# Performance work log

Hardware: AMD Instinct MI355X
Metric: run time of the kernel (lower is better)

The kernel has to match this reference:

```python
import jax, jax.numpy as jnp
import numpy as np

B, L, C = 4, 2048, 1024

def setup_inputs() -> dict:
    key = jax.random.key(0)
    k1, k2, k3 = jax.random.split(key, 3)
    net_in = jax.random.normal(k1, (B, L, C), dtype=jnp.float32)
    # torch Linear weights stored as (out, in); we keep that convention
    w_qkv = jax.random.normal(k2, (3 * C, C), dtype=jnp.float32) * (1.0 / np.sqrt(C))
    w_out = jax.random.normal(k3, (C, C), dtype=jnp.float32) * (1.0 / np.sqrt(C))
    return {"net_in": net_in, "w_qkv": w_qkv, "w_out": w_out}

def reference(net_in, w_qkv, w_out):
    Bc, Lc, Cc = net_in.shape
    qkv = jnp.einsum('blc,dc->bld', net_in, w_qkv)  # (B, L, 3C)
    q, k, v = jnp.split(qkv, 3, axis=-1)
    attn = jnp.einsum('bqc,bkc->bqk', q, k) / jnp.sqrt(jnp.float32(Cc))
    causal = jnp.tril(jnp.ones((Lc, Lc), dtype=bool))
    attn = jnp.where(causal[None, :, :], attn, -jnp.inf)
    attn = jax.nn.softmax(attn, axis=-1)
    out = jnp.einsum('bqk,bkc->bqc', attn, v)
    return jnp.einsum('blc,dc->bld', out, w_out)
```

## Files before the change

kernel.cpp:

```cpp
#include <hip/hip_runtime.h>
#include <hip/hip_bf16.h>
#include <cstdint>
#include <cstddef>

typedef __hip_bfloat16 bf16;
typedef float  floatx4 __attribute__((ext_vector_type(4)));
typedef __bf16 bf16x8  __attribute__((ext_vector_type(8)));

typedef __attribute__((address_space(1))) void as1_void;
typedef __attribute__((address_space(3))) void as3_void;

constexpr int Bn = 4, Ln = 2048, Cn = 1024;

__device__ __forceinline__ void store_one(float* p, float v) { *p = v; }
__device__ __forceinline__ void store_one(bf16*  p, float v) { *p = __float2bfloat16(v); }

#define BAR()    asm volatile("s_barrier" ::: "memory")
#define VMCNT2() asm volatile("s_waitcnt vmcnt(2)" ::: "memory")
#define VMCNT0() asm volatile("s_waitcnt vmcnt(0)" ::: "memory")
#define SCHEDB() __builtin_amdgcn_sched_barrier(0)
#define STAGE(gp, off) \
    __builtin_amdgcn_global_load_lds((const as1_void*)(gp), (as3_void*)(smem + (off)), 16, 0, 0)

template <typename OutT>
__device__ __forceinline__ void gemm256(
    const bf16* __restrict__ A, const bf16* __restrict__ B, OutT* __restrict__ C,
    int m0, int n0, int Keff, int lda, int ldb, int ldc, float cscale)
{
    __shared__ __align__(16) char smem[131072];

    const int tid  = threadIdx.x;
    const int lane = tid & 63;
    const int quad = lane >> 4;
    const int lr   = lane & 15;
    const int wave = tid >> 6;
    const int wm   = (wave >> 2) * 128;
    const int wn   = (wave & 3) * 64;

    floatx4 acc[8][4];
#pragma unroll
    for (int i = 0; i < 8; ++i)
#pragma unroll
        for (int j = 0; j < 4; ++j) { floatx4 z = {0.f, 0.f, 0.f, 0.f}; acc[i][j] = z; }

    const int srow = tid >> 3;
    const int sx   = (tid & 7) ^ (srow & 7);
    const bf16* gA = A + (size_t)(m0 + srow) * lda + sx * 8;
    const bf16* gB = B + (size_t)(n0 + srow) * ldb + sx * 8;
    const int wuni = __builtin_amdgcn_readfirstlane((tid & 0x1C0) * 16);

    const int aoff = (wm + lr) * 64;
    const int boff = (wn + lr) * 64;
    const int s0   = (quad ^ (lr & 7)) * 8;

    const int NT = Keff >> 6;

    STAGE(gB,            32768 + 0 * 8192 + wuni);
    STAGE(gB + 64  * ldb, 32768 + 1 * 8192 + wuni);
    STAGE(gB + 128 * ldb, 32768 + 2 * 8192 + wuni);
    STAGE(gB + 192 * ldb, 32768 + 3 * 8192 + wuni);
    STAGE(gA,                     0 * 8192 + wuni);
    STAGE(gA + 128 * lda,         2 * 8192 + wuni);
    STAGE(gA + 64  * lda,         1 * 8192 + wuni);
    STAGE(gA + 192 * lda,         3 * 8192 + wuni);
    VMCNT2();
    BAR();

#define LDA4(MB, SK) do { _Pragma("unroll") for (int ii = 0; ii < 4; ++ii) \
        a[ii] = *(const bf16x8*)(As + aoff + ((MB) * 4 + ii) * 1024 + (SK)); } while (0)
#define LDB4(SK) do { _Pragma("unroll") for (int nn = 0; nn < 4; ++nn) \
        b[nn] = *(const bf16x8*)(Bs + boff + nn * 1024 + (SK)); } while (0)
#define MFMA16(MB) do { _Pragma("unroll") for (int ii = 0; ii < 4; ++ii) { \
        _Pragma("unroll") for (int nn = 0; nn < 4; ++nn) \
            acc[(MB) * 4 + ii][nn] = __builtin_amdgcn_mfma_f32_16x16x32_bf16( \
                a[ii], b[nn], acc[(MB) * 4 + ii][nn], 0, 0, 0); } } while (0)

    for (int t = 0; t < NT; ++t) {
        const bf16* As = (const bf16*)(smem + (t & 1) * 65536);
        const bf16* Bs = (const bf16*)(smem + (t & 1) * 65536 + 32768);
        const int  wl  = ((t + 1) & 1) * 65536;
        const int  kn  = (t + 1) << 6;
        const bool more = (t + 1 < NT);
        bf16x8 a[4], b[4];

        LDB4(s0);
        LDA4(0, s0);
        if (more) {
            STAGE(gB + kn,            wl + 32768 + 0 * 8192 + wuni);
            STAGE(gB + kn + 64 * ldb, wl + 32768 + 1 * 8192 + wuni);
        }
        BAR(); SCHEDB();
        __builtin_amdgcn_s_setprio(1);
        MFMA16(0);
        __builtin_amdgcn_s_setprio(0);
        SCHEDB();
        if (more) VMCNT2(); else VMCNT0();
        BAR();

        LDA4(1, s0);
        if (more) {
            STAGE(gB + kn + 128 * ldb, wl + 32768 + 2 * 8192 + wuni);
            STAGE(gB + kn + 192 * ldb, wl + 32768 + 3 * 8192 + wuni);
        }
        BAR(); SCHEDB();
        __builtin_amdgcn_s_setprio(1);
        MFMA16(1);
        __builtin_amdgcn_s_setprio(0);
        SCHEDB();
        BAR();

        LDB4(s0 ^ 32);
        LDA4(0, s0 ^ 32);
        if (more) {
            STAGE(gA + kn,             wl + 0 * 8192 + wuni);
            STAGE(gA + kn + 128 * lda, wl + 2 * 8192 + wuni);
        }
        BAR(); SCHEDB();
        __builtin_amdgcn_s_setprio(1);
        MFMA16(0);
        __builtin_amdgcn_s_setprio(0);
        SCHEDB();
        BAR();

        LDA4(1, s0 ^ 32);
        if (more) {
            STAGE(gA + kn + 64  * lda, wl + 1 * 8192 + wuni);
            STAGE(gA + kn + 192 * lda, wl + 3 * 8192 + wuni);
        }
        BAR(); SCHEDB();
        __builtin_amdgcn_s_setprio(1);
        MFMA16(1);
        __builtin_amdgcn_s_setprio(0);
        SCHEDB();
        if (more) VMCNT2();
        BAR();
    }
#undef LDA4
#undef LDB4
#undef MFMA16

#pragma unroll
    for (int mi = 0; mi < 8; ++mi) {
        const int row = m0 + wm + mi * 16 + quad * 4;
#pragma unroll
        for (int n = 0; n < 4; ++n) {
            const int col = n0 + wn + n * 16 + lr;
            OutT* cp = C + (size_t)row * ldc + col;
#pragma unroll
            for (int r = 0; r < 4; ++r)
                store_one(cp + (size_t)r * ldc, acc[mi][n][r] * cscale);
        }
    }
}

__global__ __launch_bounds__(512, 2)
void g1_qk(const bf16* __restrict__ Xb, const bf16* __restrict__ Wqkb,
           bf16* __restrict__ QK)
{
    const int i = blockIdx.x;
    const int j = i >> 3;
    const int mt = (i & 7) * 4 + (j & 3);
    const int nt = j >> 2;
    gemm256<bf16>(Xb, Wqkb, QK, mt * 256, nt * 256, 1024, 1024, 1024, 2048, 1.0f);
}

__global__ __launch_bounds__(512, 2)
void g2_s_w2(const bf16* __restrict__ QK, const bf16* __restrict__ Wob,
             const bf16* __restrict__ WvT, bf16* __restrict__ S,
             bf16* __restrict__ W2)
{
    const int i = blockIdx.x;
    if (i < 144) {
        const int b = (i & 7) >> 1;
        const int t = (i >> 3) * 2 + (i & 1);
        int ti = (int)((sqrtf(8.f * t + 1.f) - 1.f) * 0.5f);
        while ((ti + 1) * (ti + 2) / 2 <= t) ++ti;
        while (ti * (ti + 1) / 2 > t) --ti;
        const int tj = t - ti * (ti + 1) / 2;
        const bf16* Aq = QK + (size_t)b * Ln * 2048;
        const bf16* Bk = Aq + 1024;
        bf16* Sb = S + (size_t)b * Ln * Ln;
        gemm256<bf16>(Aq, Bk, Sb, ti * 256, tj * 256, 1024, 2048, 2048, Ln, 0.03125f);
    } else {
        const int j = i - 144;
        gemm256<bf16>(Wob, WvT, W2, (j & 3) * 256, (j >> 2) * 256, 1024, 1024, 1024, 1024, 1.0f);
    }
}

__device__ __forceinline__ float waveMax(float x) {
#pragma unroll
    for (int o = 32; o > 0; o >>= 1) x = fmaxf(x, __shfl_xor(x, o, 64));
    return x;
}
__device__ __forceinline__ float waveSum(float x) {
#pragma unroll
    for (int o = 32; o > 0; o >>= 1) x += __shfl_xor(x, o, 64);
    return x;
}

__device__ void softmax_rows(bf16* __restrict__ S, int row0)
{
    const int wave = threadIdx.x >> 6, lane = threadIdx.x & 63;
    for (int it8 = 0; it8 < 8; ++it8) {
        const int row = row0 + wave * 8 + it8;
        const int q = row & (Ln - 1);
        bf16* Srow = S + (size_t)row * Ln;
        const int kmax = ((q >> 7) + 1) << 7;
        const int nv = (kmax + 511) >> 9;
        float x[4][8];
        float m = -1e30f;
        for (int it = 0; it < nv; ++it) {
            int c0 = it * 512 + lane * 8;
            bf16x8 v = *(const bf16x8*)(Srow + c0);
#pragma unroll
            for (int e = 0; e < 8; ++e) {
                float f = (float)v[e];
                f = (c0 + e <= q) ? f : -1e30f;
                x[it][e] = f;
                m = fmaxf(m, f);
            }
        }
        m = waveMax(m);
        float s = 0.f;
        for (int it = 0; it < nv; ++it)
#pragma unroll
            for (int e = 0; e < 8; ++e) {
                float ex = (x[it][e] > -1e29f) ? __expf(x[it][e] - m) : 0.f;
                x[it][e] = ex;
                s += ex;
            }
        s = waveSum(s);
        const float inv = 1.f / s;
        for (int it = 0; it < nv; ++it) {
            bf16x8 o;
#pragma unroll
            for (int e = 0; e < 8; ++e) o[e] = (__bf16)(x[it][e] * inv);
            *(bf16x8*)(Srow + it * 512 + lane * 8) = o;
        }
    }
}

__global__ __launch_bounds__(512, 2)
void g3_vwt_sm(const bf16* __restrict__ W2, const bf16* __restrict__ Xb,
               bf16* __restrict__ VWT, bf16* __restrict__ S)
{
    const int i = blockIdx.x;
    if (i < 128) {
        const int j = i >> 3;
        const int nt = (i & 7) * 4 + (j & 3);
        const int mt = j >> 2;
        gemm256<bf16>(W2, Xb, VWT, mt * 256, nt * 256, 1024, 1024, 1024, 8192, 1.0f);
    } else {
        softmax_rows(S, (i - 128) * 64);
    }
}

__global__ __launch_bounds__(512, 2)
void g4_out(const bf16* __restrict__ P, const bf16* __restrict__ VWT,
            float* __restrict__ out)
{
    const int i = blockIdx.x;
    const int b = (i & 7) >> 1, p = i & 1;
    const int q = i >> 3;
    const int mt = q >> 1, nt = p * 2 + (q & 1);
    const bf16* Pp = P + (size_t)b * Ln * Ln;
    const bf16* Bv = VWT + (size_t)b * Ln;
    float* Co = out + (size_t)b * Ln * Cn;
    gemm256<float>(Pp, Bv, Co, mt * 256, nt * 256, (mt + 1) * 256, Ln, 8192, Cn, 1.0f);
}

__global__ __launch_bounds__(256)
void cast_all(const float* __restrict__ X, const float* __restrict__ Wqkv,
              const float* __restrict__ Wo,
              bf16* __restrict__ Xb, bf16* __restrict__ Wqkb,
              bf16* __restrict__ Wob, bf16* __restrict__ WvT)
{
    int blk = blockIdx.x;
    if (blk < 11264) {
        int i = blk * 256 + threadIdx.x;
        const float* src; bf16* dst; int off;
        if (i < 2097152)                 { src = X;    dst = Xb;   off = i; }
        else if (i < 2097152 + 524288)   { src = Wqkv; dst = Wqkb; off = i - 2097152; }
        else                             { src = Wo;   dst = Wob;  off = i - 2621440; }
        float4 f = ((const float4*)src)[off];
        bf16 o0 = __float2bfloat16(f.x), o1 = __float2bfloat16(f.y);
        bf16 o2 = __float2bfloat16(f.z), o3 = __float2bfloat16(f.w);
        ushort4 u;
        u.x = *(unsigned short*)&o0; u.y = *(unsigned short*)&o1;
        u.z = *(unsigned short*)&o2; u.w = *(unsigned short*)&o3;
        *(ushort4*)(dst + (size_t)off * 4) = u;
    } else {
        __shared__ float t[32][33];
        int tt = blk - 11264;
        int c0 = (tt & 31) * 32;
        int r0 = (tt >> 5) * 32;
        const float* Wv = Wqkv + 2048 * 1024;
        int xcol = threadIdx.x & 31, y0 = threadIdx.x >> 5;
#pragma unroll
        for (int p = 0; p < 4; ++p) {
            int y = y0 + 8 * p;
            t[y][xcol] = Wv[(size_t)(r0 + y) * 1024 + c0 + xcol];
        }
        __syncthreads();
#pragma unroll
        for (int p = 0; p < 4; ++p) {
            int mloc = y0 + 8 * p;
            WvT[(size_t)(c0 + mloc) * 1024 + r0 + xcol] = __float2bfloat16(t[xcol][mloc]);
        }
    }
}

extern "C" void kernel_launch(void* const* d_in, const int* in_sizes, int n_in,
                              void* d_out, int out_size, void* d_ws, size_t ws_size,
                              hipStream_t stream)
{
    const float* X    = (const float*)d_in[0];
    const float* Wqkv = (const float*)d_in[1];
    const float* Wout = (const float*)d_in[2];
    float* out = (float*)d_out;

    char* ws = (char*)d_ws;
    const size_t MiB = 1024ull * 1024ull;
    bf16* Xb   = (bf16*)(ws + 0);
    bf16* QK   = (bf16*)(ws + 16 * MiB);
    bf16* VWT  = (bf16*)(ws + 48 * MiB);
    bf16* Sbuf = (bf16*)(ws + 64 * MiB);
    bf16* Wqkb = (bf16*)(ws + 96 * MiB);
    bf16* WvT  = (bf16*)(ws + 100 * MiB);
    bf16* Wob  = (bf16*)(ws + 102 * MiB);
    bf16* W2   = (bf16*)(ws + 104 * MiB);

    cast_all<<<dim3(12288), 256, 0, stream>>>(X, Wqkv, Wout, Xb, Wqkb, Wob, WvT);

    g1_qk<<<dim3(256), 512, 0, stream>>>(Xb, Wqkb, QK);

    g2_s_w2<<<dim3(160), 512, 0, stream>>>(QK, Wob, WvT, Sbuf, W2);

    g3_vwt_sm<<<dim3(256), 512, 0, stream>>>(W2, Xb, VWT, Sbuf);

    g4_out<<<dim3(128), 512, 0, stream>>>(Sbuf, VWT, out);
}
```

Measured before the change: 239.8 us.

## Split-K balance causal P·V GEMM with ticketed partial-sum reduction

The final causal attention-output GEMM had very unbalanced work per tile, since row tile mt has K length (mt+1)*256. It now launches 224 blocks: short rows are paired into one block, and long rows are split along K into 2-3 chunks. Chunk producers write fp32 partials to a scratch buffer that reuses the Xb region, then signal an atomic ticket; the consumer spins until the other chunks arrive and adds them in. This adds scratch traffic and a spin-wait that depends on co-residency of blocks, and tickets are reset inside the cast kernel.

```diff
diff --git a/kernel.cpp b/kernel.cpp
--- a/kernel.cpp
+++ b/kernel.cpp
@@ -22,13 +22,12 @@
 #define STAGE(gp, off) \
     __builtin_amdgcn_global_load_lds((const as1_void*)(gp), (as3_void*)(smem + (off)), 16, 0, 0)
 
-template <typename OutT>
-__device__ __forceinline__ void gemm256(
-    const bf16* __restrict__ A, const bf16* __restrict__ B, OutT* __restrict__ C,
-    int m0, int n0, int Keff, int lda, int ldb, int ldc, float cscale)
-{
-    __shared__ __align__(16) char smem[131072];
-
+__device__ __forceinline__ void gemm256_core(
+    char* __restrict__ smem,
+    const bf16* __restrict__ A, const bf16* __restrict__ B,
+    int m0, int n0, int kbeg, int kend, int lda, int ldb,
+    floatx4 (&acc)[8][4])
+{
     const int tid  = threadIdx.x;
     const int lane = tid & 63;
     const int quad = lane >> 4;
@@ -37,7 +36,6 @@
     const int wm   = (wave >> 2) * 128;
     const int wn   = (wave & 3) * 64;
 
-    floatx4 acc[8][4];
 #pragma unroll
     for (int i = 0; i < 8; ++i)
 #pragma unroll
@@ -45,17 +43,17 @@
 
     const int srow = tid >> 3;
     const int sx   = (tid & 7) ^ (srow & 7);
-    const bf16* gA = A + (size_t)(m0 + srow) * lda + sx * 8;
-    const bf16* gB = B + (size_t)(n0 + srow) * ldb + sx * 8;
+    const bf16* gA = A + (size_t)(m0 + srow) * lda + sx * 8 + kbeg;
+    const bf16* gB = B + (size_t)(n0 + srow) * ldb + sx * 8 + kbeg;
     const int wuni = __builtin_amdgcn_readfirstlane((tid & 0x1C0) * 16);
 
     const int aoff = (wm + lr) * 64;
     const int boff = (wn + lr) * 64;
     const int s0   = (quad ^ (lr & 7)) * 8;
 
-    const int NT = Keff >> 6;
-
-    STAGE(gB,            32768 + 0 * 8192 + wuni);
+    const int NT = (kend - kbeg) >> 6;
+
+    STAGE(gB,             32768 + 0 * 8192 + wuni);
     STAGE(gB + 64  * ldb, 32768 + 1 * 8192 + wuni);
     STAGE(gB + 128 * ldb, 32768 + 2 * 8192 + wuni);
     STAGE(gB + 192 * ldb, 32768 + 3 * 8192 + wuni);
@@ -138,6 +136,23 @@
 #undef LDA4
 #undef LDB4
 #undef MFMA16
+}
+
+template <typename OutT>
+__device__ __forceinline__ void gemm256(
+    char* __restrict__ smem,
+    const bf16* __restrict__ A, const bf16* __restrict__ B, OutT* __restrict__ C,
+    int m0, int n0, int kbeg, int kend, int lda, int ldb, int ldc, float cscale)
+{
+    floatx4 acc[8][4];
+    gemm256_core(smem, A, B, m0, n0, kbeg, kend, lda, ldb, acc);
+
+    const int lane = threadIdx.x & 63;
+    const int quad = lane >> 4;
+    const int lr   = lane & 15;
+    const int wave = threadIdx.x >> 6;
+    const int wm   = (wave >> 2) * 128;
+    const int wn   = (wave & 3) * 64;
 
 #pragma unroll
     for (int mi = 0; mi < 8; ++mi) {
@@ -157,11 +172,12 @@
 void g1_qk(const bf16* __restrict__ Xb, const bf16* __restrict__ Wqkb,
            bf16* __restrict__ QK)
 {
+    __shared__ __align__(16) char smem[131072];
     const int i = blockIdx.x;
     const int j = i >> 3;
     const int mt = (i & 7) * 4 + (j & 3);
     const int nt = j >> 2;
-    gemm256<bf16>(Xb, Wqkb, QK, mt * 256, nt * 256, 1024, 1024, 1024, 2048, 1.0f);
+    gemm256<bf16>(smem, Xb, Wqkb, QK, mt * 256, nt * 256, 0, 1024, 1024, 1024, 2048, 1.0f);
 }
 
 __global__ __launch_bounds__(512, 2)
@@ -169,6 +185,7 @@
              const bf16* __restrict__ WvT, bf16* __restrict__ S,
              bf16* __restrict__ W2)
 {
+    __shared__ __align__(16) char smem[131072];
     const int i = blockIdx.x;
     if (i < 144) {
         const int b = (i & 7) >> 1;
@@ -180,10 +197,10 @@
         const bf16* Aq = QK + (size_t)b * Ln * 2048;
         const bf16* Bk = Aq + 1024;
         bf16* Sb = S + (size_t)b * Ln * Ln;
-        gemm256<bf16>(Aq, Bk, Sb, ti * 256, tj * 256, 1024, 2048, 2048, Ln, 0.03125f);
+        gemm256<bf16>(smem, Aq, Bk, Sb, ti * 256, tj * 256, 0, 1024, 2048, 2048, Ln, 0.03125f);
     } else {
         const int j = i - 144;
-        gemm256<bf16>(Wob, WvT, W2, (j & 3) * 256, (j >> 2) * 256, 1024, 1024, 1024, 1024, 1.0f);
+        gemm256<bf16>(smem, Wob, WvT, W2, (j & 3) * 256, (j >> 2) * 256, 0, 1024, 1024, 1024, 1024, 1.0f);
     }
 }
 
@@ -244,38 +261,128 @@
 void g3_vwt_sm(const bf16* __restrict__ W2, const bf16* __restrict__ Xb,
                bf16* __restrict__ VWT, bf16* __restrict__ S)
 {
+    __shared__ __align__(16) char smem[131072];
     const int i = blockIdx.x;
     if (i < 128) {
         const int j = i >> 3;
         const int nt = (i & 7) * 4 + (j & 3);
         const int mt = j >> 2;
-        gemm256<bf16>(W2, Xb, VWT, mt * 256, nt * 256, 1024, 1024, 1024, 8192, 1.0f);
+        gemm256<bf16>(smem, W2, Xb, VWT, mt * 256, nt * 256, 0, 1024, 1024, 1024, 8192, 1.0f);
     } else {
         softmax_rows(S, (i - 128) * 64);
     }
 }
 
+__device__ const short jb_mt[14]   = {0, 2, 3, 3,   4, 4,   5, 5,   6, 6,    6,    7, 7,    7};
+__device__ const short jb_kb[14]   = {0, 0, 0, 512, 0, 768, 0, 768, 0, 768,  1280, 0, 768,  1536};
+__device__ const short jb_ke[14]   = {0, 768, 512, 1024, 768, 1280, 768, 1536, 768, 1280, 1792, 768, 1536, 2048};
+__device__ const short jb_role[14] = {0, 0, 2, 1,   2, 1,   2, 1,   2, 1,    1,    2, 1,    1};
+__device__ const short jb_cid[14]  = {0, 0, 0, 1,   0, 1,   0, 1,   0, 1,    2,    0, 1,    2};
+__device__ const short jb_nch[14]  = {1, 1, 2, 2,   2, 2,   2, 2,   3, 3,    3,    3, 3,    3};
+
 __global__ __launch_bounds__(512, 2)
 void g4_out(const bf16* __restrict__ P, const bf16* __restrict__ VWT,
-            float* __restrict__ out)
-{
+            float* __restrict__ out, float* __restrict__ paux,
+            int* __restrict__ tickets)
+{
+    __shared__ __align__(16) char smem[131072];
     const int i = blockIdx.x;
-    const int b = (i & 7) >> 1, p = i & 1;
+    const int r = i & 7;
+    const int b = r >> 1, p = r & 1;
     const int q = i >> 3;
-    const int mt = q >> 1, nt = p * 2 + (q & 1);
+    const int nt = p * 2 + (q & 1);
+    const int j = q >> 1;
+
     const bf16* Pp = P + (size_t)b * Ln * Ln;
     const bf16* Bv = VWT + (size_t)b * Ln;
     float* Co = out + (size_t)b * Ln * Cn;
-    gemm256<float>(Pp, Bv, Co, mt * 256, nt * 256, (mt + 1) * 256, Ln, 8192, Cn, 1.0f);
+    const int n0 = nt * 256;
+
+    if (j == 0) {
+        gemm256<float>(smem, Pp, Bv, Co, 0,   n0, 0, 256, Ln, 8192, Cn, 1.0f);
+        gemm256<float>(smem, Pp, Bv, Co, 256, n0, 0, 512, Ln, 8192, Cn, 1.0f);
+        return;
+    }
+
+    const int mt   = jb_mt[j];
+    const int kb   = jb_kb[j];
+    const int ke   = jb_ke[j];
+    const int role = jb_role[j];
+    const int m0   = mt * 256;
+
+    if (role == 0) {
+        gemm256<float>(smem, Pp, Bv, Co, m0, n0, kb, ke, Ln, 8192, Cn, 1.0f);
+        return;
+    }
+
+    floatx4 acc[8][4];
+    gemm256_core(smem, Pp, Bv, m0, n0, kb, ke, Ln, 8192, acc);
+
+    const int tid  = threadIdx.x;
+    const int lane = tid & 63;
+    const int quad = lane >> 4;
+    const int lr   = lane & 15;
+    const int wave = tid >> 6;
+    const int wm   = (wave >> 2) * 128;
+    const int wn   = (wave & 3) * 64;
+
+    const int tred = (b * 4 + nt) * 5 + (mt - 3);
+    float* slot0 = paux + ((size_t)(tred * 2) << 16);
+
+    if (role == 1) {
+        const int cid = jb_cid[j];
+        float* slot = slot0 + ((size_t)(cid - 1) << 16);
+#pragma unroll
+        for (int mi = 0; mi < 8; ++mi) {
+            const int lrow = wm + mi * 16 + quad * 4;
+#pragma unroll
+            for (int n = 0; n < 4; ++n) {
+                const int lcol = wn + n * 16 + lr;
+#pragma unroll
+                for (int rr = 0; rr < 4; ++rr)
+                    slot[(size_t)(lrow + rr) * 256 + lcol] = acc[mi][n][rr];
+            }
+        }
+        __threadfence();
+        __syncthreads();
+        if (tid == 0)
+            __hip_atomic_fetch_add(&tickets[tred], 1, __ATOMIC_RELEASE, __HIP_MEMORY_SCOPE_AGENT);
+        return;
+    }
+
+    const int nch = jb_nch[j];
+    if (tid == 0) {
+        while (__hip_atomic_load(&tickets[tred], __ATOMIC_ACQUIRE, __HIP_MEMORY_SCOPE_AGENT) < nch - 1)
+            __builtin_amdgcn_s_sleep(8);
+    }
+    __syncthreads();
+    const float* s1 = slot0 + 65536;
+#pragma unroll
+    for (int mi = 0; mi < 8; ++mi) {
+        const int lrow = wm + mi * 16 + quad * 4;
+#pragma unroll
+        for (int n = 0; n < 4; ++n) {
+            const int lcol = wn + n * 16 + lr;
+#pragma unroll
+            for (int rr = 0; rr < 4; ++rr) {
+                const size_t li = (size_t)(lrow + rr) * 256 + lcol;
+                float v = acc[mi][n][rr] + slot0[li];
+                if (nch == 3) v += s1[li];
+                Co[(size_t)(m0 + lrow + rr) * Cn + n0 + lcol] = v;
+            }
+        }
+    }
 }
 
 __global__ __launch_bounds__(256)
 void cast_all(const float* __restrict__ X, const float* __restrict__ Wqkv,
               const float* __restrict__ Wo,
               bf16* __restrict__ Xb, bf16* __restrict__ Wqkb,
-              bf16* __restrict__ Wob, bf16* __restrict__ WvT)
+              bf16* __restrict__ Wob, bf16* __restrict__ WvT,
+              int* __restrict__ tickets)
 {
     int blk = blockIdx.x;
+    if (blk == 0 && threadIdx.x < 128) tickets[threadIdx.x] = 0;
     if (blk < 11264) {
         int i = blk * 256 + threadIdx.x;
         const float* src; bf16* dst; int off;
@@ -329,8 +436,10 @@
     bf16* WvT  = (bf16*)(ws + 100 * MiB);
     bf16* Wob  = (bf16*)(ws + 102 * MiB);
     bf16* W2   = (bf16*)(ws + 104 * MiB);
-
-    cast_all<<<dim3(12288), 256, 0, stream>>>(X, Wqkv, Wout, Xb, Wqkb, Wob, WvT);
+    float* paux = (float*)(ws + 0);
+    int* tickets = (int*)(ws + 106 * MiB);
+
+    cast_all<<<dim3(12288), 256, 0, stream>>>(X, Wqkv, Wout, Xb, Wqkb, Wob, WvT, tickets);
 
     g1_qk<<<dim3(256), 512, 0, stream>>>(Xb, Wqkb, QK);
 
@@ -338,5 +447,5 @@
 
     g3_vwt_sm<<<dim3(256), 512, 0, stream>>>(W2, Xb, VWT, Sbuf);
 
-    g4_out<<<dim3(128), 512, 0, stream>>>(Sbuf, VWT, out);
-}
+    g4_out<<<dim3(224), 512, 0, stream>>>(Sbuf, VWT, out, paux, tickets);
+}
```

Result: slower. 327.3 us (+36.5%).

## Shrink GEMM tiles to 128x128 and redistribute work across more blocks

Applied to the files above, without the earlier changes.

Replaces the 256x256 GEMM tile with a 128x128 tile, using 64KB of shared memory and a simpler staging schedule that waits on all loads each k-step. Grids grow four-fold, with new tile-index swizzles, and occupancy rises to 4 blocks per CU. Softmax now runs in every g3 block after its GEMM instead of in separate blocks. The goal is better load balance and CU fill on the small causal and triangular grids, at the cost of lower operand reuse per tile and more global traffic.

```diff
diff --git a/kernel.cpp b/kernel.cpp
--- a/kernel.cpp
+++ b/kernel.cpp
@@ -16,32 +16,30 @@
 __device__ __forceinline__ void store_one(bf16*  p, float v) { *p = __float2bfloat16(v); }
 
 #define BAR()    asm volatile("s_barrier" ::: "memory")
-#define VMCNT2() asm volatile("s_waitcnt vmcnt(2)" ::: "memory")
 #define VMCNT0() asm volatile("s_waitcnt vmcnt(0)" ::: "memory")
 #define SCHEDB() __builtin_amdgcn_sched_barrier(0)
 #define STAGE(gp, off) \
     __builtin_amdgcn_global_load_lds((const as1_void*)(gp), (as3_void*)(smem + (off)), 16, 0, 0)
 
 template <typename OutT>
-__device__ __forceinline__ void gemm256(
+__device__ __forceinline__ void gemm128(
+    char* __restrict__ smem,
     const bf16* __restrict__ A, const bf16* __restrict__ B, OutT* __restrict__ C,
-    int m0, int n0, int Keff, int lda, int ldb, int ldc, float cscale)
-{
-    __shared__ __align__(16) char smem[131072];
-
+    int m0, int n0, int kend, int lda, int ldb, int ldc, float cscale)
+{
     const int tid  = threadIdx.x;
     const int lane = tid & 63;
     const int quad = lane >> 4;
     const int lr   = lane & 15;
     const int wave = tid >> 6;
-    const int wm   = (wave >> 2) * 128;
-    const int wn   = (wave & 3) * 64;
-
-    floatx4 acc[8][4];
-#pragma unroll
-    for (int i = 0; i < 8; ++i)
-#pragma unroll
-        for (int j = 0; j < 4; ++j) { floatx4 z = {0.f, 0.f, 0.f, 0.f}; acc[i][j] = z; }
+    const int wm   = (wave >> 2) * 64;
+    const int wn   = (wave & 3) * 32;
+
+    floatx4 acc[4][2];
+#pragma unroll
+    for (int i = 0; i < 4; ++i)
+#pragma unroll
+        for (int j = 0; j < 2; ++j) { floatx4 z = {0.f, 0.f, 0.f, 0.f}; acc[i][j] = z; }
 
     const int srow = tid >> 3;
     const int sx   = (tid & 7) ^ (srow & 7);
@@ -53,97 +51,82 @@
     const int boff = (wn + lr) * 64;
     const int s0   = (quad ^ (lr & 7)) * 8;
 
-    const int NT = Keff >> 6;
-
-    STAGE(gB,            32768 + 0 * 8192 + wuni);
-    STAGE(gB + 64  * ldb, 32768 + 1 * 8192 + wuni);
-    STAGE(gB + 128 * ldb, 32768 + 2 * 8192 + wuni);
-    STAGE(gB + 192 * ldb, 32768 + 3 * 8192 + wuni);
-    STAGE(gA,                     0 * 8192 + wuni);
-    STAGE(gA + 128 * lda,         2 * 8192 + wuni);
-    STAGE(gA + 64  * lda,         1 * 8192 + wuni);
-    STAGE(gA + 192 * lda,         3 * 8192 + wuni);
-    VMCNT2();
+    const int NT  = kend >> 6;
+    const int BUF = 32768;
+
+#define STG4(KN, bo) do { \
+        STAGE(gA + (KN),            (bo) + 0 * 8192 + wuni); \
+        STAGE(gA + (KN) + 64 * lda, (bo) + 1 * 8192 + wuni); \
+        STAGE(gB + (KN),            (bo) + 16384 + 0 * 8192 + wuni); \
+        STAGE(gB + (KN) + 64 * ldb, (bo) + 16384 + 1 * 8192 + wuni); } while (0)
+
+    STG4(0, 0);
+    VMCNT0();
     BAR();
 
-#define LDA4(MB, SK) do { _Pragma("unroll") for (int ii = 0; ii < 4; ++ii) \
-        a[ii] = *(const bf16x8*)(As + aoff + ((MB) * 4 + ii) * 1024 + (SK)); } while (0)
-#define LDB4(SK) do { _Pragma("unroll") for (int nn = 0; nn < 4; ++nn) \
+#define LDA2(PH, SK) do { _Pragma("unroll") for (int ii = 0; ii < 2; ++ii) \
+        a[ii] = *(const bf16x8*)(As + aoff + ((PH) * 2 + ii) * 1024 + (SK)); } while (0)
+#define LDB2(SK) do { _Pragma("unroll") for (int nn = 0; nn < 2; ++nn) \
         b[nn] = *(const bf16x8*)(Bs + boff + nn * 1024 + (SK)); } while (0)
-#define MFMA16(MB) do { _Pragma("unroll") for (int ii = 0; ii < 4; ++ii) { \
-        _Pragma("unroll") for (int nn = 0; nn < 4; ++nn) \
-            acc[(MB) * 4 + ii][nn] = __builtin_amdgcn_mfma_f32_16x16x32_bf16( \
-                a[ii], b[nn], acc[(MB) * 4 + ii][nn], 0, 0, 0); } } while (0)
+#define MFMA4(PH) do { _Pragma("unroll") for (int ii = 0; ii < 2; ++ii) { \
+        _Pragma("unroll") for (int nn = 0; nn < 2; ++nn) \
+            acc[(PH) * 2 + ii][nn] = __builtin_amdgcn_mfma_f32_16x16x32_bf16( \
+                a[ii], b[nn], acc[(PH) * 2 + ii][nn], 0, 0, 0); } } while (0)
 
     for (int t = 0; t < NT; ++t) {
-        const bf16* As = (const bf16*)(smem + (t & 1) * 65536);
-        const bf16* Bs = (const bf16*)(smem + (t & 1) * 65536 + 32768);
-        const int  wl  = ((t + 1) & 1) * 65536;
+        const bf16* As = (const bf16*)(smem + (t & 1) * BUF);
+        const bf16* Bs = (const bf16*)(smem + (t & 1) * BUF + 16384);
+        const int  wl  = ((t + 1) & 1) * BUF;
         const int  kn  = (t + 1) << 6;
         const bool more = (t + 1 < NT);
-        bf16x8 a[4], b[4];
-
-        LDB4(s0);
-        LDA4(0, s0);
-        if (more) {
-            STAGE(gB + kn,            wl + 32768 + 0 * 8192 + wuni);
-            STAGE(gB + kn + 64 * ldb, wl + 32768 + 1 * 8192 + wuni);
-        }
+        bf16x8 a[2], b[2];
+
+        LDB2(s0);
+        LDA2(0, s0);
+        if (more) STG4(kn, wl);
         BAR(); SCHEDB();
         __builtin_amdgcn_s_setprio(1);
-        MFMA16(0);
-        __builtin_amdgcn_s_setprio(0);
-        SCHEDB();
-        if (more) VMCNT2(); else VMCNT0();
-        BAR();
-
-        LDA4(1, s0);
-        if (more) {
-            STAGE(gB + kn + 128 * ldb, wl + 32768 + 2 * 8192 + wuni);
-            STAGE(gB + kn + 192 * ldb, wl + 32768 + 3 * 8192 + wuni);
-        }
-        BAR(); SCHEDB();
-        __builtin_amdgcn_s_setprio(1);
-        MFMA16(1);
+        MFMA4(0);
         __builtin_amdgcn_s_setprio(0);
         SCHEDB();
         BAR();
 
-        LDB4(s0 ^ 32);
-        LDA4(0, s0 ^ 32);
-        if (more) {
-            STAGE(gA + kn,             wl + 0 * 8192 + wuni);
-            STAGE(gA + kn + 128 * lda, wl + 2 * 8192 + wuni);
-        }
+        LDA2(1, s0);
         BAR(); SCHEDB();
         __builtin_amdgcn_s_setprio(1);
-        MFMA16(0);
+        MFMA4(1);
         __builtin_amdgcn_s_setprio(0);
         SCHEDB();
         BAR();
 
-        LDA4(1, s0 ^ 32);
-        if (more) {
-            STAGE(gA + kn + 64  * lda, wl + 1 * 8192 + wuni);
-            STAGE(gA + kn + 192 * lda, wl + 3 * 8192 + wuni);
-        }
+        LDB2(s0 ^ 32);
+        LDA2(0, s0 ^ 32);
         BAR(); SCHEDB();
         __builtin_amdgcn_s_setprio(1);
-        MFMA16(1);
+        MFMA4(0);
         __builtin_amdgcn_s_setprio(0);
         SCHEDB();
-        if (more) VMCNT2();
         BAR();
-    }
-#undef LDA4
-#undef LDB4
-#undef MFMA16
-
-#pragma unroll
-    for (int mi = 0; mi < 8; ++mi) {
+
+        LDA2(1, s0 ^ 32);
+        BAR(); SCHEDB();
+        __builtin_amdgcn_s_setprio(1);
+        MFMA4(1);
+        __builtin_amdgcn_s_setprio(0);
+        SCHEDB();
+        if (more) VMCNT0();
+        BAR();
+    }
+#undef LDA2
+#undef LDB2
+#undef MFMA4
+#undef STG4
+
+#pragma unroll
+    for (int mi = 0; mi < 4; ++mi) {
         const int row = m0 + wm + mi * 16 + quad * 4;
 #pragma unroll
-        for (int n = 0; n < 4; ++n) {
+        for (int n = 0; n < 2; ++n) {
             const int col = n0 + wn + n * 16 + lr;
             OutT* cp = C + (size_t)row * ldc + col;
 #pragma unroll
@@ -153,26 +136,30 @@
     }
 }
 
-__global__ __launch_bounds__(512, 2)
+__global__ __launch_bounds__(512, 4)
 void g1_qk(const bf16* __restrict__ Xb, const bf16* __restrict__ Wqkb,
            bf16* __restrict__ QK)
 {
+    __shared__ __align__(16) char smem[65536];
     const int i = blockIdx.x;
-    const int j = i >> 3;
-    const int mt = (i & 7) * 4 + (j & 3);
-    const int nt = j >> 2;
-    gemm256<bf16>(Xb, Wqkb, QK, mt * 256, nt * 256, 1024, 1024, 1024, 2048, 1.0f);
-}
-
-__global__ __launch_bounds__(512, 2)
+    const int x = i & 7;
+    const int r = i >> 3;
+    const int mt = x * 8 + (r & 7);
+    const int nt = r >> 3;
+    gemm128<bf16>(smem, Xb, Wqkb, QK, mt * 128, nt * 128, 1024, 1024, 1024, 2048, 1.0f);
+}
+
+__global__ __launch_bounds__(512, 4)
 void g2_s_w2(const bf16* __restrict__ QK, const bf16* __restrict__ Wob,
              const bf16* __restrict__ WvT, bf16* __restrict__ S,
              bf16* __restrict__ W2)
 {
+    __shared__ __align__(16) char smem[65536];
     const int i = blockIdx.x;
-    if (i < 144) {
+    if (i < 544) {
         const int b = (i & 7) >> 1;
-        const int t = (i >> 3) * 2 + (i & 1);
+        const int p = i & 1;
+        const int t = (i >> 3) * 2 + p;
         int ti = (int)((sqrtf(8.f * t + 1.f) - 1.f) * 0.5f);
         while ((ti + 1) * (ti + 2) / 2 <= t) ++ti;
         while (ti * (ti + 1) / 2 > t) --ti;
@@ -180,10 +167,10 @@
         const bf16* Aq = QK + (size_t)b * Ln * 2048;
         const bf16* Bk = Aq + 1024;
         bf16* Sb = S + (size_t)b * Ln * Ln;
-        gemm256<bf16>(Aq, Bk, Sb, ti * 256, tj * 256, 1024, 2048, 2048, Ln, 0.03125f);
+        gemm128<bf16>(smem, Aq, Bk, Sb, ti * 128, tj * 128, 1024, 2048, 2048, Ln, 0.03125f);
     } else {
-        const int j = i - 144;
-        gemm256<bf16>(Wob, WvT, W2, (j & 3) * 256, (j >> 2) * 256, 1024, 1024, 1024, 1024, 1.0f);
+        const int j = i - 544;
+        gemm128<bf16>(smem, Wob, WvT, W2, (j >> 3) * 128, (j & 7) * 128, 1024, 1024, 1024, 1024, 1.0f);
     }
 }
 
@@ -198,11 +185,11 @@
     return x;
 }
 
-__device__ void softmax_rows(bf16* __restrict__ S, int row0)
+__device__ void softmax_rows16(bf16* __restrict__ S, int i)
 {
     const int wave = threadIdx.x >> 6, lane = threadIdx.x & 63;
-    for (int it8 = 0; it8 < 8; ++it8) {
-        const int row = row0 + wave * 8 + it8;
+    for (int it2 = 0; it2 < 2; ++it2) {
+        const int row = i + 512 * (wave * 2 + it2);
         const int q = row & (Ln - 1);
         bf16* Srow = S + (size_t)row * Ln;
         const int kmax = ((q >> 7) + 1) << 7;
@@ -240,33 +227,34 @@
     }
 }
 
-__global__ __launch_bounds__(512, 2)
+__global__ __launch_bounds__(512, 4)
 void g3_vwt_sm(const bf16* __restrict__ W2, const bf16* __restrict__ Xb,
                bf16* __restrict__ VWT, bf16* __restrict__ S)
 {
+    __shared__ __align__(16) char smem[65536];
     const int i = blockIdx.x;
-    if (i < 128) {
-        const int j = i >> 3;
-        const int nt = (i & 7) * 4 + (j & 3);
-        const int mt = j >> 2;
-        gemm256<bf16>(W2, Xb, VWT, mt * 256, nt * 256, 1024, 1024, 1024, 8192, 1.0f);
-    } else {
-        softmax_rows(S, (i - 128) * 64);
-    }
-}
-
-__global__ __launch_bounds__(512, 2)
+    const int x = i & 7;
+    const int r = i >> 3;
+    const int nt = x * 8 + (r & 7);
+    const int mh = r >> 3;
+    gemm128<bf16>(smem, W2, Xb, VWT, mh * 128, nt * 128, 1024, 1024, 1024, 8192, 1.0f);
+    softmax_rows16(S, i);
+}
+
+__global__ __launch_bounds__(512, 4)
 void g4_out(const bf16* __restrict__ P, const bf16* __restrict__ VWT,
             float* __restrict__ out)
 {
+    __shared__ __align__(16) char smem[65536];
     const int i = blockIdx.x;
     const int b = (i & 7) >> 1, p = i & 1;
-    const int q = i >> 3;
-    const int mt = q >> 1, nt = p * 2 + (q & 1);
+    const int nt = p * 4 + ((i >> 3) & 3);
+    const int mh = 15 - (i >> 5);
+
     const bf16* Pp = P + (size_t)b * Ln * Ln;
     const bf16* Bv = VWT + (size_t)b * Ln;
     float* Co = out + (size_t)b * Ln * Cn;
-    gemm256<float>(Pp, Bv, Co, mt * 256, nt * 256, (mt + 1) * 256, Ln, 8192, Cn, 1.0f);
+    gemm128<float>(smem, Pp, Bv, Co, mh * 128, nt * 128, (mh + 1) * 128, Ln, 8192, Cn, 1.0f);
 }
 
 __global__ __launch_bounds__(256)
@@ -332,11 +320,11 @@
 
     cast_all<<<dim3(12288), 256, 0, stream>>>(X, Wqkv, Wout, Xb, Wqkb, Wob, WvT);
 
-    g1_qk<<<dim3(256), 512, 0, stream>>>(Xb, Wqkb, QK);
-
-    g2_s_w2<<<dim3(160), 512, 0, stream>>>(QK, Wob, WvT, Sbuf, W2);
-
-    g3_vwt_sm<<<dim3(256), 512, 0, stream>>>(W2, Xb, VWT, Sbuf);
-
-    g4_out<<<dim3(128), 512, 0, stream>>>(Sbuf, VWT, out);
-}
+    g1_qk<<<dim3(1024), 512, 0, stream>>>(Xb, Wqkb, QK);
+
+    g2_s_w2<<<dim3(608), 512, 0, stream>>>(QK, Wob, WvT, Sbuf, W2);
+
+    g3_vwt_sm<<<dim3(512), 512, 0, stream>>>(W2, Xb, VWT, Sbuf);
+
+    g4_out<<<dim3(512), 512, 0, stream>>>(Sbuf, VWT, out);
+}
```

New measurement: 228.2 us. 4.8% less time.
